# Kernel optimization log

Measured on AMD Instinct MI355X. Metric: run time of the kernel, lower is better.

Reference implementation:

```python
import jax, jax.numpy as jnp
import numpy as np

H = 2            # num attention heads (hardcoded in Model)
D = 128          # head dim = hidden // H
HID = H * D      # hidden_channels = 256
SQRT_D = float(np.sqrt(D))


def _seg_softmax(logits, seg, n):
    # softmax over incoming edges per destination node; logits [E,H]
    m = jax.ops.segment_max(logits, seg, num_segments=n)
    m = jnp.where(jnp.isfinite(m), m, 0.0)
    e = jnp.exp(logits - m[seg])
    s = jax.ops.segment_sum(e, seg, num_segments=n)
    return e / (s[seg] + 1e-16)


def _hgt_dst(q_t, k_s, v_s, src, dst, Wk_rel, Wv_rel, p_rel, n_t):
    # per-edge-type relation projections of source keys/values: [N_s,H,D]
    k_e = jnp.einsum('nhd,hde->nhe', k_s, Wk_rel)[src]   # [E,H,D]
    v_e = jnp.einsum('nhd,hde->nhe', v_s, Wv_rel)[src]   # [E,H,D]
    logits = jnp.einsum('ehd,ehd->eh', q_t[dst], k_e) * p_rel / SQRT_D  # [E,H]
    a = _seg_softmax(logits, dst, n_t)
    agg = jax.ops.segment_sum(a[:, :, None] * v_e, dst, num_segments=n_t)
    return agg.reshape(n_t, HID)


def _forward(x_author, x_paper, edge_w_src, edge_w_dst, edge_b_src, edge_b_dst,
             input_nodes, W_in_a, b_in_a, W_in_p, b_in_p, Wkqv_a, bkqv_a,
             Wkqv_p, bkqv_p, Wk_rel_w, Wv_rel_w, Wk_rel_b, Wv_rel_b, p_w, p_b,
             Wout_a, bout_a, Wout_p, bout_p, skip_a, skip_p, W_dec, b_dec):
    # per-node-type input projection + relu (GNNEncoder.lin_dict)
    xa = jax.nn.relu(x_author @ W_in_a + b_in_a)   # [Na,HID]
    xp = jax.nn.relu(x_paper @ W_in_p + b_in_p)    # [Np,HID]
    Na, Np = xa.shape[0], xp.shape[0]
    # HGTConv: fused k/q/v projections per node type
    kqv_a = (xa @ Wkqv_a + bkqv_a).reshape(Na, 3, H, D)
    kqv_p = (xp @ Wkqv_p + bkqv_p).reshape(Np, 3, H, D)
    k_a, q_a, v_a = kqv_a[:, 0], kqv_a[:, 1], kqv_a[:, 2]
    k_p, q_p, v_p = kqv_p[:, 0], kqv_p[:, 1], kqv_p[:, 2]
    # ('author','writes','paper'): dst=paper; ('paper','written_by','author'): dst=author
    out_p = _hgt_dst(q_p, k_a, v_a, edge_w_src, edge_w_dst, Wk_rel_w, Wv_rel_w, p_w, Np)
    out_a = _hgt_dst(q_a, k_p, v_p, edge_b_src, edge_b_dst, Wk_rel_b, Wv_rel_b, p_b, Na)
    # output projection (gelu then linear) + gated skip connection
    out_a = jax.nn.gelu(out_a, approximate=False) @ Wout_a + bout_a
    out_p = jax.nn.gelu(out_p, approximate=False) @ Wout_p + bout_p
    ga = jax.nn.sigmoid(skip_a)
    gp = jax.nn.sigmoid(skip_p)
    za = ga * out_a + (1.0 - ga) * xa
    zp = gp * out_p + (1.0 - gp) * xp  # computed for faithfulness (unused by decoder)
    del zp
    # NodeDecoder: sigmoid(lin(z[input]) @ z_all^T)
    z_in = za[input_nodes] @ W_dec + b_dec   # [NI,HID]
    return jax.nn.sigmoid(z_in @ za.T)       # [NI,Na]


def setup_inputs() -> dict:
    key = jax.random.key(0)
    ks = jax.random.split(key, 20)
    Na = Np = 50000
    Din = 128
    E = 800000
    NI = 512
    g_in = 1.0 / np.sqrt(Din)
    g_h = 1.0 / np.sqrt(HID)
    g_d = 1.0 / np.sqrt(D)
    r = jax.random.normal
    return dict(
        x_author=r(ks[0], (Na, Din), jnp.float32),
        x_paper=r(ks[1], (Np, Din), jnp.float32),
        edge_w_src=jax.random.randint(ks[2], (E,), 0, Na),
        edge_w_dst=jax.random.randint(ks[3], (E,), 0, Np),
        edge_b_src=jax.random.randint(ks[4], (E,), 0, Np),
        edge_b_dst=jax.random.randint(ks[5], (E,), 0, Na),
        input_nodes=jax.random.randint(ks[6], (NI,), 0, Na),
        W_in_a=r(ks[7], (Din, HID)) * g_in, b_in_a=jnp.zeros((HID,)),
        W_in_p=r(ks[8], (Din, HID)) * g_in, b_in_p=jnp.zeros((HID,)),
        Wkqv_a=r(ks[9], (HID, 3 * HID)) * g_h, bkqv_a=jnp.zeros((3 * HID,)),
        Wkqv_p=r(ks[10], (HID, 3 * HID)) * g_h, bkqv_p=jnp.zeros((3 * HID,)),
        Wk_rel_w=r(ks[11], (H, D, D)) * g_d,
        Wv_rel_w=r(ks[12], (H, D, D)) * g_d,
        Wk_rel_b=r(ks[13], (H, D, D)) * g_d,
        Wv_rel_b=r(ks[14], (H, D, D)) * g_d,
        p_w=jnp.ones((H,)), p_b=jnp.ones((H,)),
        Wout_a=r(ks[15], (HID, HID)) * g_h, bout_a=jnp.zeros((HID,)),
        Wout_p=r(ks[16], (HID, HID)) * g_h, bout_p=jnp.zeros((HID,)),
        skip_a=jnp.array(1.0), skip_p=jnp.array(1.0),
        W_dec=r(ks[17], (HID, HID)) * g_h, b_dec=jnp.zeros((HID,)),
    )


def reference(x_author, x_paper, edge_w_src, edge_w_dst, edge_b_src, edge_b_dst,
              input_nodes, W_in_a, b_in_a, W_in_p, b_in_p, Wkqv_a, bkqv_a,
              Wkqv_p, bkqv_p, Wk_rel_w, Wv_rel_w, Wk_rel_b, Wv_rel_b, p_w, p_b,
              Wout_a, bout_a, Wout_p, bout_p, skip_a, skip_p, W_dec, b_dec):
    return _forward(x_author, x_paper, edge_w_src, edge_w_dst, edge_b_src,
                    edge_b_dst, input_nodes, W_in_a, b_in_a, W_in_p, b_in_p,
                    Wkqv_a, bkqv_a, Wkqv_p, bkqv_p, Wk_rel_w, Wv_rel_w,
                    Wk_rel_b, Wv_rel_b, p_w, p_b, Wout_a, bout_a, Wout_p,
                    bout_p, skip_a, skip_p, W_dec, b_dec)
```

## Files before the change

kernel.cpp:

```cpp
#include <hip/hip_runtime.h>
#include <math.h>

#define HID 256

typedef __bf16 bf16_t;
typedef __attribute__((ext_vector_type(8))) __bf16 bf16x8;
typedef __attribute__((ext_vector_type(4))) __bf16 bf16x4;
typedef __attribute__((ext_vector_type(4))) float f32x4;

__device__ __forceinline__ float gelu_f(float x){
  return 0.5f * x * (1.0f + erff(x * 0.70710678118654752440f));
}

__device__ __forceinline__ void gload16(const void* g, void* l){
  __builtin_amdgcn_global_load_lds(
      (const __attribute__((address_space(1))) unsigned int*)g,
      (__attribute__((address_space(3))) unsigned int*)l, 16, 0, 0);
}

__global__ __launch_bounds__(256) void mfma_gemm_k(
    const void* __restrict__ A, int lda,
    const bf16_t* __restrict__ Bt, int ldb,
    const float* __restrict__ bias,
    void* __restrict__ Cout, int ldc,
    int M, int N, int K,
    int mode, int a_gelu, int a_f32,
    const int* __restrict__ a_rows,
    const float* __restrict__ pvec,
    const bf16_t* __restrict__ skipx,
    const float* __restrict__ skip_gate)
{
  __shared__ bf16_t As[128*64];
  __shared__ bf16_t Bs[128*64];
  const int t = threadIdx.x;
  const int wave = t >> 6, lane = t & 63;
  const int quad = lane >> 4, l16 = lane & 15;
  const int row0 = blockIdx.y*128, col0 = blockIdx.x*128;
  const int R = (wave>>1)*64, Cb = (wave&1)*64;
  const int lrow = lane >> 3;
  const int schunk = (lane & 7) ^ lrow;
  const bool a_direct = (!a_f32 && !a_gelu);
  f32x4 acc[4][4] = {};

  for (int k0 = 0; k0 < K; k0 += 64){
    if (a_direct){
#pragma unroll
      for (int i = 0; i < 4; i++){
        int r0 = wave*32 + i*8;
        int gr = row0 + r0 + lrow;
        int rr = gr < M ? gr : M-1;
        int ar = a_rows ? a_rows[rr] : rr;
        gload16((const bf16_t*)A + (long long)ar*lda + k0 + schunk*8, As + r0*64);
      }
    } else {
#pragma unroll
      for (int i = 0; i < 4; i++){
        int id = t + i*256;
        int r = id >> 3, c4 = id & 7;
        int gr = row0 + r;
        bf16x8 v = {};
        if (gr < M){
          if (a_f32){
            const float* p = (const float*)A + (long long)gr*lda + k0 + c4*8;
            float4 f0 = *(const float4*)p;
            float4 f1 = *(const float4*)(p + 4);
            v[0]=(bf16_t)f0.x; v[1]=(bf16_t)f0.y; v[2]=(bf16_t)f0.z; v[3]=(bf16_t)f0.w;
            v[4]=(bf16_t)f1.x; v[5]=(bf16_t)f1.y; v[6]=(bf16_t)f1.z; v[7]=(bf16_t)f1.w;
          } else {
            v = *(const bf16x8*)((const bf16_t*)A + (long long)gr*lda + k0 + c4*8);
#pragma unroll
            for (int j = 0; j < 8; j++) v[j] = (bf16_t)gelu_f((float)v[j]);
          }
        }
        *(bf16x8*)(As + r*64 + ((c4 ^ (r&7))*8)) = v;
      }
    }
#pragma unroll
    for (int i = 0; i < 4; i++){
      int r0 = wave*32 + i*8;
      int gc = col0 + r0 + lrow;
      int rc = gc < N ? gc : N-1;
      gload16(Bt + (long long)rc*ldb + k0 + schunk*8, Bs + r0*64);
    }
    __syncthreads();
#pragma unroll
    for (int kk = 0; kk < 64; kk += 32){
      const int cb = quad + (kk >> 3);
      bf16x8 af[4], bfr[4];
#pragma unroll
      for (int i = 0; i < 4; i++){
        int row = R + 16*i + l16;
        af[i]  = *(const bf16x8*)(As + row*64 + ((cb ^ (row&7))*8));
      }
#pragma unroll
      for (int j = 0; j < 4; j++){
        int row = Cb + 16*j + l16;
        bfr[j] = *(const bf16x8*)(Bs + row*64 + ((cb ^ (row&7))*8));
      }
#pragma unroll
      for (int i = 0; i < 4; i++)
#pragma unroll
        for (int j = 0; j < 4; j++)
          acc[i][j] = __builtin_amdgcn_mfma_f32_16x16x32_bf16(af[i], bfr[j], acc[i][j], 0, 0, 0);
    }
    __syncthreads();
  }

  float gate = 0.f;
  if (mode == 3) gate = 1.f/(1.f + expf(-(*skip_gate)));
#pragma unroll
  for (int i = 0; i < 4; i++){
#pragma unroll
    for (int j = 0; j < 4; j++){
#pragma unroll
      for (int r = 0; r < 4; r++){
        int gr = row0 + R + 16*i + quad*4 + r;
        int gc = col0 + Cb + 16*j + l16;
        if (gr >= M || gc >= N) continue;
        float v = acc[i][j][r] + (bias ? bias[gc] : 0.f);
        if (mode == 1) v = fmaxf(v, 0.f);
        else if (mode == 2) v *= pvec[gc >> 7] * 0.08838834764831845f;
        else if (mode == 3) v = gate*v + (1.f - gate)*(float)skipx[(long long)gr*HID + gc];
        if (mode == 4) ((float*)Cout)[(long long)gr*ldc + gc] = 1.f/(1.f + expf(-v));
        else ((bf16_t*)Cout)[(long long)gr*ldc + gc] = (bf16_t)v;
      }
    }
  }
}

struct TW { const float* W; bf16_t* out; int lda; int K; int N; };

__global__ __launch_bounds__(256) void prep_weights_k(TW w0, TW w1, TW w2, TW w3, TW w4){
  TW tw;
  switch (blockIdx.z){
    case 0: tw = w0; break; case 1: tw = w1; break; case 2: tw = w2; break;
    case 3: tw = w3; break; default: tw = w4; break;
  }
  __shared__ float tile[32][33];
  int bx = blockIdx.x*32, by = blockIdx.y*32;
  if (by >= tw.K || bx >= tw.N) return;
  int tx = threadIdx.x, ty = threadIdx.y;
  for (int i = 0; i < 32; i += 8){
    int k = by + ty + i, n = bx + tx;
    tile[ty+i][tx] = (k < tw.K && n < tw.N) ? tw.W[(long long)k*tw.lda + n] : 0.f;
  }
  __syncthreads();
  for (int i = 0; i < 32; i += 8){
    int n = bx + ty + i, k = by + tx;
    if (n < tw.N && k < tw.K) tw.out[(long long)n*tw.K + k] = (bf16_t)tile[tx][ty+i];
  }
}

__global__ __launch_bounds__(256) void prep_fold_k(
    const float* __restrict__ Wkqv_p, const float* __restrict__ bkqv_p,
    const float* __restrict__ Wk_rel, const float* __restrict__ Wv_rel,
    bf16_t* __restrict__ Wkvt, float* __restrict__ bkv)
{
  int np = blockIdx.x;
  int kv = np >> 8, h = (np >> 7) & 1, n = np & 127;
  int off = kv*512 + h*128;
  const float* rel = (kv ? Wv_rel : Wk_rel) + h*128*128 + n;
  __shared__ float relcol[128];
  int t = threadIdx.x;
  if (t < 128) relcol[t] = rel[t*128];
  __syncthreads();
  int m = t;
  const float* wp = Wkqv_p + (long long)m*768 + off;
  float acc = 0.f;
#pragma unroll 8
  for (int k = 0; k < 128; k++) acc += wp[k] * relcol[k];
  Wkvt[(long long)np*256 + m] = (bf16_t)acc;
  if (t == 0){
    float b = 0.f;
    for (int k = 0; k < 128; k++) b += bkqv_p[off + k] * relcol[k];
    bkv[np] = b;
  }
}

__global__ void hist_k(const int* __restrict__ dst, int E, int* __restrict__ deg){
  int i = blockIdx.x*256 + threadIdx.x;
  if (i < E) atomicAdd(&deg[dst[i]], 1);
}

__global__ __launch_bounds__(256) void partial_sum_k(
    const int* __restrict__ deg, int n, int* __restrict__ part)
{
  __shared__ int sdata[4];
  int i = blockIdx.x*256 + threadIdx.x;
  int v = (i < n) ? deg[i] : 0;
#pragma unroll
  for (int o = 32; o; o >>= 1) v += __shfl_xor(v, o);
  int lane = threadIdx.x & 63, wid = threadIdx.x >> 6;
  if (lane == 0) sdata[wid] = v;
  __syncthreads();
  if (threadIdx.x == 0) part[blockIdx.x] = sdata[0]+sdata[1]+sdata[2]+sdata[3];
}

__global__ __launch_bounds__(256) void scan_part_k(
    int* __restrict__ part, int nb, int* __restrict__ total_out)
{
  __shared__ int ws[4]; __shared__ int tot;
  int t = threadIdx.x;
  int v = (t < nb) ? part[t] : 0;
  int lane = t & 63, wid = t >> 6;
  int x = v;
#pragma unroll
  for (int o = 1; o < 64; o <<= 1){ int y = __shfl_up(x, o); if (lane >= o) x += y; }
  if (lane == 63) ws[wid] = x;
  __syncthreads();
  if (t == 0){ int s = 0; for (int i = 0; i < 4; i++){ int tmp = ws[i]; ws[i] = s; s += tmp; } tot = s; }
  __syncthreads();
  int excl = x - v + ws[wid];
  if (t < nb) part[t] = excl;
  if (t == 0) *total_out = tot;
}

__global__ __launch_bounds__(256) void scan_offs_k(
    const int* __restrict__ deg, int n, const int* __restrict__ part,
    int* __restrict__ offs, int* __restrict__ cursor)
{
  __shared__ int ws[4];
  int t = threadIdx.x;
  int i = blockIdx.x*256 + t;
  int v = (i < n) ? deg[i] : 0;
  int lane = t & 63, wid = t >> 6;
  int x = v;
#pragma unroll
  for (int o = 1; o < 64; o <<= 1){ int y = __shfl_up(x, o); if (lane >= o) x += y; }
  if (lane == 63) ws[wid] = x;
  __syncthreads();
  int pre = 0;
  for (int k = 0; k < wid; k++) pre += ws[k];
  if (i < n){ int o = part[blockIdx.x] + x - v + pre; offs[i] = o; cursor[i] = o; }
}

__global__ void scatter_k(const int* __restrict__ src, const int* __restrict__ dst, int E,
                          int* __restrict__ cursor, int* __restrict__ esrc){
  int i = blockIdx.x*256 + threadIdx.x;
  if (i < E){
    int s = src[i], d = dst[i];
    int p = atomicAdd(&cursor[d], 1);
    esrc[p] = s;
  }
}

__global__ __launch_bounds__(256) void attn_fused_k(
    const bf16_t* __restrict__ q, const bf16_t* __restrict__ keve,
    const int* __restrict__ offs, const int* __restrict__ esrc,
    int Na, bf16_t* __restrict__ agg)
{
  int gid = blockIdx.x*256 + threadIdx.x;
  int dst = gid >> 6, lane = gid & 63;
  if (dst >= Na) return;
  const int hl = lane & 31;
  const int half = lane >> 5;
  bf16x8 qv = *(const bf16x8*)(q + (size_t)dst*256 + hl*8);
  float qf[8];
#pragma unroll
  for (int j = 0; j < 8; j++) qf[j] = (float)qv[j];
  int beg = offs[dst], end = offs[dst+1];
  int cnt = end - beg;
  int cap = cnt < 64 ? cnt : 64;
  int myidx = 0;
  if (cnt > 0) myidx = esrc[beg + (lane < cnt ? lane : cnt - 1)];
  float n[8] = {};
  float den = 0.f;

  int npairs = cap >> 1;
  int it = 0;
  for (; it + 4 <= npairs; it += 4){
    int es0 = __shfl(myidx, 2*it     + half);
    int es1 = __shfl(myidx, 2*it + 2 + half);
    int es2 = __shfl(myidx, 2*it + 4 + half);
    int es3 = __shfl(myidx, 2*it + 6 + half);
    const bf16_t* r0 = keve + ((size_t)(unsigned)es0 << 9);
    const bf16_t* r1 = keve + ((size_t)(unsigned)es1 << 9);
    const bf16_t* r2 = keve + ((size_t)(unsigned)es2 << 9);
    const bf16_t* r3 = keve + ((size_t)(unsigned)es3 << 9);
    bf16x8 k0 = *(const bf16x8*)(r0 + hl*8);
    bf16x8 k1 = *(const bf16x8*)(r1 + hl*8);
    bf16x8 k2 = *(const bf16x8*)(r2 + hl*8);
    bf16x8 k3 = *(const bf16x8*)(r3 + hl*8);
    bf16x8 v0 = *(const bf16x8*)(r0 + 256 + hl*8);
    bf16x8 v1 = *(const bf16x8*)(r1 + 256 + hl*8);
    bf16x8 v2 = *(const bf16x8*)(r2 + 256 + hl*8);
    bf16x8 v3 = *(const bf16x8*)(r3 + 256 + hl*8);
    float p0 = 0.f, p1 = 0.f, p2 = 0.f, p3 = 0.f;
#pragma unroll
    for (int j = 0; j < 8; j++){
      p0 += qf[j]*(float)k0[j];
      p1 += qf[j]*(float)k1[j];
      p2 += qf[j]*(float)k2[j];
      p3 += qf[j]*(float)k3[j];
    }
#pragma unroll
    for (int o = 1; o <= 8; o <<= 1){
      p0 += __shfl_xor(p0, o);
      p1 += __shfl_xor(p1, o);
      p2 += __shfl_xor(p2, o);
      p3 += __shfl_xor(p3, o);
    }
    float w0 = __expf(p0), w1 = __expf(p1), w2 = __expf(p2), w3 = __expf(p3);
#pragma unroll
    for (int j = 0; j < 8; j++)
      n[j] += w0*(float)v0[j] + w1*(float)v1[j] + w2*(float)v2[j] + w3*(float)v3[j];
    den += w0 + w1 + w2 + w3;
  }
  for (; it < npairs; ++it){
    int es = __shfl(myidx, 2*it + half);
    const bf16_t* row = keve + ((size_t)(unsigned)es << 9);
    bf16x8 kv = *(const bf16x8*)(row + hl*8);
    bf16x8 vv = *(const bf16x8*)(row + 256 + hl*8);
    float p = qf[0]*(float)kv[0] + qf[1]*(float)kv[1]
            + qf[2]*(float)kv[2] + qf[3]*(float)kv[3]
            + qf[4]*(float)kv[4] + qf[5]*(float)kv[5]
            + qf[6]*(float)kv[6] + qf[7]*(float)kv[7];
    p += __shfl_xor(p, 1); p += __shfl_xor(p, 2);
    p += __shfl_xor(p, 4); p += __shfl_xor(p, 8);
    float wgt = __expf(p);
#pragma unroll
    for (int j = 0; j < 8; j++) n[j] += wgt*(float)vv[j];
    den += wgt;
  }
  if (cap & 1){
    int es = __shfl(myidx, cap - 1);
    const bf16_t* row = keve + ((size_t)(unsigned)es << 9);
    bf16x8 kv = *(const bf16x8*)(row + hl*8);
    bf16x8 vv = *(const bf16x8*)(row + 256 + hl*8);
    float p = qf[0]*(float)kv[0] + qf[1]*(float)kv[1]
            + qf[2]*(float)kv[2] + qf[3]*(float)kv[3]
            + qf[4]*(float)kv[4] + qf[5]*(float)kv[5]
            + qf[6]*(float)kv[6] + qf[7]*(float)kv[7];
    p += __shfl_xor(p, 1); p += __shfl_xor(p, 2);
    p += __shfl_xor(p, 4); p += __shfl_xor(p, 8);
    float wgt = (half == 0) ? __expf(p) : 0.f;
#pragma unroll
    for (int j = 0; j < 8; j++) n[j] += wgt*(float)vv[j];
    den += wgt;
  }
  for (int i = beg + 64; i < end; i += 2){
    int e2 = i + half;
    int es = esrc[(e2 < end) ? e2 : i];
    const bf16_t* row = keve + ((size_t)(unsigned)es << 9);
    bf16x8 kv = *(const bf16x8*)(row + hl*8);
    bf16x8 vv = *(const bf16x8*)(row + 256 + hl*8);
    float p = qf[0]*(float)kv[0] + qf[1]*(float)kv[1]
            + qf[2]*(float)kv[2] + qf[3]*(float)kv[3]
            + qf[4]*(float)kv[4] + qf[5]*(float)kv[5]
            + qf[6]*(float)kv[6] + qf[7]*(float)kv[7];
    p += __shfl_xor(p, 1); p += __shfl_xor(p, 2);
    p += __shfl_xor(p, 4); p += __shfl_xor(p, 8);
    float wgt = (e2 < end) ? __expf(p) : 0.f;
#pragma unroll
    for (int j = 0; j < 8; j++) n[j] += wgt*(float)vv[j];
    den += wgt;
  }
  den += __shfl_xor(den, 32);
#pragma unroll
  for (int j = 0; j < 8; j++) n[j] += __shfl_xor(n[j], 32);
  if (half == 0){
    float r = 1.f/(den + 1e-16f);
    bf16x8 o;
#pragma unroll
    for (int j = 0; j < 8; j++) o[j] = (bf16_t)(n[j]*r);
    *(bf16x8*)(agg + (size_t)dst*256 + hl*8) = o;
  }
}

extern "C" void kernel_launch(void* const* d_in, const int* in_sizes, int n_in,
                              void* d_out, int out_size, void* d_ws, size_t ws_size,
                              hipStream_t stream)
{
  (void)n_in; (void)out_size; (void)ws_size;
  const float* x_author    = (const float*)d_in[0];
  const float* x_paper     = (const float*)d_in[1];
  const int*   eb_src      = (const int*)d_in[4];
  const int*   eb_dst      = (const int*)d_in[5];
  const int*   input_nodes = (const int*)d_in[6];
  const float* W_in_a  = (const float*)d_in[7];
  const float* b_in_a  = (const float*)d_in[8];
  const float* W_in_p  = (const float*)d_in[9];
  const float* b_in_p  = (const float*)d_in[10];
  const float* Wkqv_a  = (const float*)d_in[11];
  const float* bkqv_a  = (const float*)d_in[12];
  const float* Wkqv_p  = (const float*)d_in[13];
  const float* bkqv_p  = (const float*)d_in[14];
  const float* Wk_rel_b= (const float*)d_in[17];
  const float* Wv_rel_b= (const float*)d_in[18];
  const float* p_b     = (const float*)d_in[20];
  const float* Wout_a  = (const float*)d_in[21];
  const float* bout_a  = (const float*)d_in[22];
  const float* skip_a  = (const float*)d_in[25];
  const float* W_dec   = (const float*)d_in[27];
  const float* b_dec   = (const float*)d_in[28];

  const int Na = in_sizes[0] / 128;
  const int Np = in_sizes[1] / 128;
  const int E  = in_sizes[4];
  const int NI = in_sizes[6];

  char* w = (char*)d_ws;
  auto alloc = [&](size_t bytes)->void*{
    void* p = (void*)w; w += (bytes + 255) & ~(size_t)255; return p;
  };
  bf16_t* xa_bf = (bf16_t*)alloc((size_t)Na*HID*2);
  bf16_t* xp_bf = (bf16_t*)alloc((size_t)Np*HID*2);
  bf16_t* qb    = (bf16_t*)alloc((size_t)Na*HID*2);
  bf16_t* aggb  = (bf16_t*)alloc((size_t)Na*HID*2);
  bf16_t* zin   = (bf16_t*)alloc((size_t)NI*HID*2);
  bf16_t* Wt_in_a = (bf16_t*)alloc(128*HID*2);
  bf16_t* Wt_in_p = (bf16_t*)alloc(128*HID*2);
  bf16_t* Wt_q    = (bf16_t*)alloc(HID*HID*2);
  bf16_t* Wt_out  = (bf16_t*)alloc(HID*HID*2);
  bf16_t* Wt_dec  = (bf16_t*)alloc(HID*HID*2);
  bf16_t* Wkvt    = (bf16_t*)alloc((size_t)512*HID*2);
  float*  bkv     = (float*)alloc(512*4);
  int* deg    = (int*)alloc((size_t)Na*4);
  int* offs   = (int*)alloc((size_t)(Na+1)*4);
  int* cursor = (int*)alloc((size_t)Na*4);
  int* part   = (int*)alloc(1024);
  int* esrc   = (int*)alloc((size_t)E*4);

  bf16_t* keve = (bf16_t*)d_out;
  bf16_t* zab  = qb;

  dim3 blk(256);

  TW tw0 = { W_in_a,       Wt_in_a, 256, 128, 256 };
  TW tw1 = { W_in_p,       Wt_in_p, 256, 128, 256 };
  TW tw2 = { Wkqv_a + 256, Wt_q,    768, 256, 256 };
  TW tw3 = { Wout_a,       Wt_out,  256, 256, 256 };
  TW tw4 = { W_dec,        Wt_dec,  256, 256, 256 };
  prep_weights_k<<<dim3(8,8,5), dim3(32,8), 0, stream>>>(tw0, tw1, tw2, tw3, tw4);
  prep_fold_k<<<512, blk, 0, stream>>>(Wkqv_p, bkqv_p, Wk_rel_b, Wv_rel_b, Wkvt, bkv);

  dim3 gNa(2, (Na+127)/128);
  dim3 gNp(2, (Np+127)/128);
  mfma_gemm_k<<<gNa, blk, 0, stream>>>(x_author, 128, Wt_in_a, 128, b_in_a, xa_bf, HID,
      Na, 256, 128, 1, 0, 1, nullptr, nullptr, nullptr, nullptr);
  mfma_gemm_k<<<gNp, blk, 0, stream>>>(x_paper, 128, Wt_in_p, 128, b_in_p, xp_bf, HID,
      Np, 256, 128, 1, 0, 1, nullptr, nullptr, nullptr, nullptr);
  mfma_gemm_k<<<gNa, blk, 0, stream>>>(xa_bf, HID, Wt_q, HID, bkqv_a + 256, qb, HID,
      Na, 256, 256, 2, 0, 0, nullptr, p_b, nullptr, nullptr);
  mfma_gemm_k<<<dim3(4,(Np+127)/128), blk, 0, stream>>>(xp_bf, HID, Wkvt, HID, bkv, keve, 512,
      Np, 512, 256, 0, 0, 0, nullptr, nullptr, nullptr, nullptr);
  hipMemsetAsync(deg, 0, (size_t)Na*4, stream);
  hist_k<<<(E+255)/256, blk, 0, stream>>>(eb_dst, E, deg);
  int nb = (Na+255)/256;
  partial_sum_k<<<nb, blk, 0, stream>>>(deg, Na, part);
  scan_part_k<<<1, blk, 0, stream>>>(part, nb, offs+Na);
  scan_offs_k<<<nb, blk, 0, stream>>>(deg, Na, part, offs, cursor);
  scatter_k<<<(E+255)/256, blk, 0, stream>>>(eb_src, eb_dst, E, cursor, esrc);
  attn_fused_k<<<(Na+3)/4, blk, 0, stream>>>(qb, keve, offs, esrc, Na, aggb);
  mfma_gemm_k<<<gNa, blk, 0, stream>>>(aggb, HID, Wt_out, HID, bout_a, zab, HID,
      Na, 256, 256, 3, 1, 0, nullptr, nullptr, xa_bf, skip_a);
  mfma_gemm_k<<<dim3(2,(NI+127)/128), blk, 0, stream>>>(zab, HID, Wt_dec, HID, b_dec, zin, HID,
      NI, 256, 256, 0, 0, 0, input_nodes, nullptr, nullptr, nullptr);
  mfma_gemm_k<<<dim3((Na+127)/128, (NI+127)/128), blk, 0, stream>>>(zin, HID, zab, HID, nullptr,
      (float*)d_out, Na, NI, Na, 256, 4, 0, 0, nullptr, nullptr, nullptr, nullptr);
}
```

Before: 762.5 us.

## Batch independent GEMMs and edge histogram/scatter into shared launches

```diff
diff --git a/kernel.cpp b/kernel.cpp
--- a/kernel.cpp
+++ b/kernel.cpp
@@ -18,39 +18,42 @@
       (__attribute__((address_space(3))) unsigned int*)l, 16, 0, 0);
 }
 
-__global__ __launch_bounds__(256) void mfma_gemm_k(
-    const void* __restrict__ A, int lda,
-    const bf16_t* __restrict__ Bt, int ldb,
-    const float* __restrict__ bias,
-    void* __restrict__ Cout, int ldc,
-    int M, int N, int K,
-    int mode, int a_gelu, int a_f32,
-    const int* __restrict__ a_rows,
-    const float* __restrict__ pvec,
-    const bf16_t* __restrict__ skipx,
-    const float* __restrict__ skip_gate)
-{
+struct GArgs {
+  const void* A; int lda;
+  const bf16_t* Bt; int ldb;
+  const float* bias;
+  void* Cout; int ldc;
+  int M, N, K;
+  int mode, a_gelu, a_f32;
+  const int* a_rows;
+  const float* pvec;
+  const bf16_t* skipx;
+  const float* skip_gate;
+};
+
+__device__ void gemm_body(const GArgs& g){
   __shared__ bf16_t As[128*64];
   __shared__ bf16_t Bs[128*64];
+  const int row0 = blockIdx.y*128, col0 = blockIdx.x*128;
+  if (row0 >= g.M || col0 >= g.N) return;
   const int t = threadIdx.x;
   const int wave = t >> 6, lane = t & 63;
   const int quad = lane >> 4, l16 = lane & 15;
-  const int row0 = blockIdx.y*128, col0 = blockIdx.x*128;
   const int R = (wave>>1)*64, Cb = (wave&1)*64;
   const int lrow = lane >> 3;
   const int schunk = (lane & 7) ^ lrow;
-  const bool a_direct = (!a_f32 && !a_gelu);
+  const bool a_direct = (!g.a_f32 && !g.a_gelu);
   f32x4 acc[4][4] = {};
 
-  for (int k0 = 0; k0 < K; k0 += 64){
+  for (int k0 = 0; k0 < g.K; k0 += 64){
     if (a_direct){
 #pragma unroll
       for (int i = 0; i < 4; i++){
         int r0 = wave*32 + i*8;
         int gr = row0 + r0 + lrow;
-        int rr = gr < M ? gr : M-1;
-        int ar = a_rows ? a_rows[rr] : rr;
-        gload16((const bf16_t*)A + (long long)ar*lda + k0 + schunk*8, As + r0*64);
+        int rr = gr < g.M ? gr : g.M-1;
+        int ar = g.a_rows ? g.a_rows[rr] : rr;
+        gload16((const bf16_t*)g.A + (long long)ar*g.lda + k0 + schunk*8, As + r0*64);
       }
     } else {
 #pragma unroll
@@ -59,15 +62,15 @@
         int r = id >> 3, c4 = id & 7;
         int gr = row0 + r;
         bf16x8 v = {};
-        if (gr < M){
-          if (a_f32){
-            const float* p = (const float*)A + (long long)gr*lda + k0 + c4*8;
+        if (gr < g.M){
+          if (g.a_f32){
+            const float* p = (const float*)g.A + (long long)gr*g.lda + k0 + c4*8;
             float4 f0 = *(const float4*)p;
             float4 f1 = *(const float4*)(p + 4);
             v[0]=(bf16_t)f0.x; v[1]=(bf16_t)f0.y; v[2]=(bf16_t)f0.z; v[3]=(bf16_t)f0.w;
             v[4]=(bf16_t)f1.x; v[5]=(bf16_t)f1.y; v[6]=(bf16_t)f1.z; v[7]=(bf16_t)f1.w;
           } else {
-            v = *(const bf16x8*)((const bf16_t*)A + (long long)gr*lda + k0 + c4*8);
+            v = *(const bf16x8*)((const bf16_t*)g.A + (long long)gr*g.lda + k0 + c4*8);
 #pragma unroll
             for (int j = 0; j < 8; j++) v[j] = (bf16_t)gelu_f((float)v[j]);
           }
@@ -79,8 +82,8 @@
     for (int i = 0; i < 4; i++){
       int r0 = wave*32 + i*8;
       int gc = col0 + r0 + lrow;
-      int rc = gc < N ? gc : N-1;
-      gload16(Bt + (long long)rc*ldb + k0 + schunk*8, Bs + r0*64);
+      int rc = gc < g.N ? gc : g.N-1;
+      gload16(g.Bt + (long long)rc*g.ldb + k0 + schunk*8, Bs + r0*64);
     }
     __syncthreads();
 #pragma unroll
@@ -107,7 +110,7 @@
   }
 
   float gate = 0.f;
-  if (mode == 3) gate = 1.f/(1.f + expf(-(*skip_gate)));
+  if (g.mode == 3) gate = 1.f/(1.f + expf(-(*g.skip_gate)));
 #pragma unroll
   for (int i = 0; i < 4; i++){
 #pragma unroll
@@ -116,16 +119,33 @@
       for (int r = 0; r < 4; r++){
         int gr = row0 + R + 16*i + quad*4 + r;
         int gc = col0 + Cb + 16*j + l16;
-        if (gr >= M || gc >= N) continue;
-        float v = acc[i][j][r] + (bias ? bias[gc] : 0.f);
-        if (mode == 1) v = fmaxf(v, 0.f);
-        else if (mode == 2) v *= pvec[gc >> 7] * 0.08838834764831845f;
-        else if (mode == 3) v = gate*v + (1.f - gate)*(float)skipx[(long long)gr*HID + gc];
-        if (mode == 4) ((float*)Cout)[(long long)gr*ldc + gc] = 1.f/(1.f + expf(-v));
-        else ((bf16_t*)Cout)[(long long)gr*ldc + gc] = (bf16_t)v;
+        if (gr >= g.M || gc >= g.N) continue;
+        float v = acc[i][j][r] + (g.bias ? g.bias[gc] : 0.f);
+        if (g.mode == 1) v = fmaxf(v, 0.f);
+        else if (g.mode == 2) v *= g.pvec[gc >> 7] * 0.08838834764831845f;
+        else if (g.mode == 3) v = gate*v + (1.f - gate)*(float)g.skipx[(long long)gr*HID + gc];
+        if (g.mode == 4) ((float*)g.Cout)[(long long)gr*g.ldc + gc] = 1.f/(1.f + expf(-v));
+        else ((bf16_t*)g.Cout)[(long long)gr*g.ldc + gc] = (bf16_t)v;
       }
     }
   }
+}
+
+__global__ __launch_bounds__(256) void gemm_batch_k(
+    GArgs g0, GArgs g1, int eop,
+    const int* __restrict__ e_a, const int* __restrict__ e_b, int E,
+    int* __restrict__ e_c, int* __restrict__ e_d)
+{
+  if (blockIdx.z == 2){
+    int nblk = gridDim.x*gridDim.y;
+    int bid  = blockIdx.y*gridDim.x + blockIdx.x;
+    for (int i = bid*256 + threadIdx.x; i < E; i += nblk*256){
+      if (eop == 1) atomicAdd(&e_c[e_a[i]], 1);
+      else { int s = e_a[i], d = e_b[i]; int p = atomicAdd(&e_c[d], 1); e_d[p] = s; }
+    }
+    return;
+  }
+  gemm_body(blockIdx.z ? g1 : g0);
 }
 
 struct TW { const float* W; bf16_t* out; int lda; int K; int N; };
@@ -177,11 +197,6 @@
   }
 }
 
-__global__ void hist_k(const int* __restrict__ dst, int E, int* __restrict__ deg){
-  int i = blockIdx.x*256 + threadIdx.x;
-  if (i < E) atomicAdd(&deg[dst[i]], 1);
-}
-
 __global__ __launch_bounds__(256) void partial_sum_k(
     const int* __restrict__ deg, int n, int* __restrict__ part)
 {
@@ -232,16 +247,6 @@
   int pre = 0;
   for (int k = 0; k < wid; k++) pre += ws[k];
   if (i < n){ int o = part[blockIdx.x] + x - v + pre; offs[i] = o; cursor[i] = o; }
-}
-
-__global__ void scatter_k(const int* __restrict__ src, const int* __restrict__ dst, int E,
-                          int* __restrict__ cursor, int* __restrict__ esrc){
-  int i = blockIdx.x*256 + threadIdx.x;
-  if (i < E){
-    int s = src[i], d = dst[i];
-    int p = atomicAdd(&cursor[d], 1);
-    esrc[p] = s;
-  }
 }
 
 __global__ __launch_bounds__(256) void attn_fused_k(
@@ -433,29 +438,43 @@
   TW tw4 = { W_dec,        Wt_dec,  256, 256, 256 };
   prep_weights_k<<<dim3(8,8,5), dim3(32,8), 0, stream>>>(tw0, tw1, tw2, tw3, tw4);
   prep_fold_k<<<512, blk, 0, stream>>>(Wkqv_p, bkqv_p, Wk_rel_b, Wv_rel_b, Wkvt, bkv);
-
-  dim3 gNa(2, (Na+127)/128);
-  dim3 gNp(2, (Np+127)/128);
-  mfma_gemm_k<<<gNa, blk, 0, stream>>>(x_author, 128, Wt_in_a, 128, b_in_a, xa_bf, HID,
-      Na, 256, 128, 1, 0, 1, nullptr, nullptr, nullptr, nullptr);
-  mfma_gemm_k<<<gNp, blk, 0, stream>>>(x_paper, 128, Wt_in_p, 128, b_in_p, xp_bf, HID,
-      Np, 256, 128, 1, 0, 1, nullptr, nullptr, nullptr, nullptr);
-  mfma_gemm_k<<<gNa, blk, 0, stream>>>(xa_bf, HID, Wt_q, HID, bkqv_a + 256, qb, HID,
-      Na, 256, 256, 2, 0, 0, nullptr, p_b, nullptr, nullptr);
-  mfma_gemm_k<<<dim3(4,(Np+127)/128), blk, 0, stream>>>(xp_bf, HID, Wkvt, HID, bkv, keve, 512,
-      Np, 512, 256, 0, 0, 0, nullptr, nullptr, nullptr, nullptr);
   hipMemsetAsync(deg, 0, (size_t)Na*4, stream);
-  hist_k<<<(E+255)/256, blk, 0, stream>>>(eb_dst, E, deg);
+
+  GArgs gz = {};
+
+  GArgs ga = { x_author, 128, Wt_in_a, 128, b_in_a, xa_bf, HID,
+               Na, 256, 128, 1, 0, 1, nullptr, nullptr, nullptr, nullptr };
+  GArgs gp = { x_paper,  128, Wt_in_p, 128, b_in_p, xp_bf, HID,
+               Np, 256, 128, 1, 0, 1, nullptr, nullptr, nullptr, nullptr };
+  gemm_batch_k<<<dim3(2, (Na+127)/128, 3), blk, 0, stream>>>(
+      ga, gp, 1, eb_dst, nullptr, E, deg, nullptr);
+
   int nb = (Na+255)/256;
   partial_sum_k<<<nb, blk, 0, stream>>>(deg, Na, part);
   scan_part_k<<<1, blk, 0, stream>>>(part, nb, offs+Na);
   scan_offs_k<<<nb, blk, 0, stream>>>(deg, Na, part, offs, cursor);
-  scatter_k<<<(E+255)/256, blk, 0, stream>>>(eb_src, eb_dst, E, cursor, esrc);
+
+  GArgs gq = { xa_bf, HID, Wt_q, HID, bkqv_a + 256, qb, HID,
+               Na, 256, 256, 2, 0, 0, nullptr, p_b, nullptr, nullptr };
+  GArgs gk = { xp_bf, HID, Wkvt, HID, bkv, keve, 512,
+               Np, 512, 256, 0, 0, 0, nullptr, nullptr, nullptr, nullptr };
+  gemm_batch_k<<<dim3(4, (Np+127)/128, 3), blk, 0, stream>>>(
+      gq, gk, 2, eb_src, eb_dst, E, cursor, esrc);
+
   attn_fused_k<<<(Na+3)/4, blk, 0, stream>>>(qb, keve, offs, esrc, Na, aggb);
-  mfma_gemm_k<<<gNa, blk, 0, stream>>>(aggb, HID, Wt_out, HID, bout_a, zab, HID,
-      Na, 256, 256, 3, 1, 0, nullptr, nullptr, xa_bf, skip_a);
-  mfma_gemm_k<<<dim3(2,(NI+127)/128), blk, 0, stream>>>(zab, HID, Wt_dec, HID, b_dec, zin, HID,
-      NI, 256, 256, 0, 0, 0, input_nodes, nullptr, nullptr, nullptr);
-  mfma_gemm_k<<<dim3((Na+127)/128, (NI+127)/128), blk, 0, stream>>>(zin, HID, zab, HID, nullptr,
-      (float*)d_out, Na, NI, Na, 256, 4, 0, 0, nullptr, nullptr, nullptr, nullptr);
-}
+
+  GArgs gza = { aggb, HID, Wt_out, HID, bout_a, zab, HID,
+                Na, 256, 256, 3, 1, 0, nullptr, nullptr, xa_bf, skip_a };
+  gemm_batch_k<<<dim3(2, (Na+127)/128, 1), blk, 0, stream>>>(
+      gza, gz, 0, nullptr, nullptr, 0, nullptr, nullptr);
+
+  GArgs gzin = { zab, HID, Wt_dec, HID, b_dec, zin, HID,
+                 NI, 256, 256, 0, 0, 0, input_nodes, nullptr, nullptr, nullptr };
+  gemm_batch_k<<<dim3(2, (NI+127)/128, 1), blk, 0, stream>>>(
+      gzin, gz, 0, nullptr, nullptr, 0, nullptr, nullptr);
+
+  GArgs gout = { zin, HID, zab, HID, nullptr, (float*)d_out, Na,
+                 NI, Na, 256, 4, 0, 0, nullptr, nullptr, nullptr, nullptr };
+  gemm_batch_k<<<dim3((Na+127)/128, (NI+127)/128, 1), blk, 0, stream>>>(
+      gout, gz, 0, nullptr, nullptr, 0, nullptr, nullptr);
+}
```

Measured after the change: 701.6 us. -8.0%, faster.
